# Kernel optimization log

Hardware: AMD Instinct MI355X
Metric: run time of the kernel (lower is better)

## Reference

```python
import jax, jax.numpy as jnp
import numpy as np

B, T = 512, 8192
DT = jnp.float32(1e-3)


def setup_inputs() -> dict:
    key = jax.random.key(0)
    k1, k2, k3, k4 = jax.random.split(key, 4)
    # scale noise so the 8192-step linear recurrence stays well-conditioned
    xicovs = jax.random.normal(k1, (B, T, 2, 2), jnp.float32) * 0.05
    dy = jax.random.normal(k2, (B, T, 2), jnp.float32) * 0.05
    coeffs_A = jax.random.uniform(k3, (2, 2), jnp.float32, -0.05, 0.05)  # 'uniform' init kernel
    C = jax.random.normal(k4, (2, 2), jnp.float32)
    return {"xicovs": xicovs, "dy": dy, "coeffs_A": coeffs_A, "C": C}


def reference(xicovs, dy, coeffs_A, C):
    # xicovs: [B,T,2,2], dy: [B,T,2]
    Bv = xicovs.shape[0]
    # initial state [1,0] broadcast over batch
    x0 = jnp.broadcast_to(jnp.array([1.0, 0.0], jnp.float32), (Bv, 2))
    xi_t = jnp.swapaxes(xicovs, 0, 1)  # [T,B,2,2]
    dy_t = jnp.swapaxes(dy, 0, 1)      # [T,B,2]

    def step(x, inp):
        xic, dyt = inp  # [B,2,2], [B,2]
        # cell emits C @ x_prev * dt
        out = jnp.einsum('ij,bj->bi', C, x) * DT
        A_minus_xiC = coeffs_A - jnp.einsum('bij,jk->bik', xic, C)  # [B,2,2]
        dx = jnp.einsum('bij,bj->bi', A_minus_xiC, x) * DT + jnp.einsum('bij,bj->bi', xic, dyt)
        return x + dx, out

    _, outs = jax.lax.scan(step, x0, (xi_t, dy_t))  # outs: [T,B,2]
    return jnp.swapaxes(outs, 0, 1)  # [B,T,2] (return_sequences=True)
```

## Files before the change

### kernel.cpp

```cpp
#include <hip/hip_runtime.h>


#define B_   512
#define T_   8192
#define LPT  8
#define NT   1024
#define NB   2
static_assert(NT * LPT == T_, "one block covers one batch");

#define SLICE_F4 128

struct Aff { float m00, m01, m10, m11, v0, v1; };

__device__ __forceinline__ Aff aff_compose(const Aff& L, const Aff& E) {
    Aff r;
    r.m00 = L.m00*E.m00 + L.m01*E.m10;
    r.m01 = L.m00*E.m01 + L.m01*E.m11;
    r.m10 = L.m10*E.m00 + L.m11*E.m10;
    r.m11 = L.m10*E.m01 + L.m11*E.m11;
    r.v0  = L.m00*E.v0  + L.m01*E.v1 + L.v0;
    r.v1  = L.m10*E.v0  + L.m11*E.v1 + L.v1;
    return r;
}

__device__ __forceinline__ Aff aff_identity() {
    Aff r; r.m00 = 1.f; r.m01 = 0.f; r.m10 = 0.f; r.m11 = 1.f; r.v0 = 0.f; r.v1 = 0.f;
    return r;
}

#define STEP_MAP(i, S)                                                  \
    {                                                                   \
        const float4 x4 = a[i];                                         \
        const float dyx = ((i)&1) ? d[(i)>>1].z : d[(i)>>1].x;          \
        const float dyy = ((i)&1) ? d[(i)>>1].w : d[(i)>>1].y;          \
        (S).m00 = i00 - (x4.x*cd00 + x4.y*cd10);                        \
        (S).m01 = i01 - (x4.x*cd01 + x4.y*cd11);                        \
        (S).m10 = i10 - (x4.z*cd00 + x4.w*cd10);                        \
        (S).m11 = i11 - (x4.z*cd01 + x4.w*cd11);                        \
        (S).v0  = x4.x*dyx + x4.y*dyy;                                  \
        (S).v1  = x4.z*dyx + x4.w*dyy;                                  \
    }

template<bool PREFETCH_DY>
__device__ __forceinline__ void process_batch(
    float4 (&t)[8], float4 (&u)[4],
    float4* __restrict__ slice, float4* __restrict__ lds4,
    const int lane, const int wave,
    const float cd00, const float cd01, const float cd10, const float cd11,
    const float i00, const float i01, const float i10, const float i11,
    float4* __restrict__ ow,
    const float4* __restrict__ dw_next, float4 (&u_next)[4])
{
    float4 a[LPT];
    #pragma unroll
    for (int r = 0; r < 4; ++r) {
        #pragma unroll
        for (int jj = 0; jj < 2; ++jj) {
            int j = 2*r + jj;
            int f = j*64 + lane;
            int rel = (f >> 3) & 15;
            slice[rel*8 + ((lane & 7) ^ (rel & 7))] = t[j];
        }
        if ((lane >> 4) == r) {
            int rel = lane & 15;
            #pragma unroll
            for (int s = 0; s < LPT; ++s)
                a[s] = slice[rel*8 + (s ^ (rel & 7))];
        }
    }

    float4 d[4];
    #pragma unroll
    for (int r = 0; r < 2; ++r) {
        #pragma unroll
        for (int jj = 0; jj < 2; ++jj) {
            int j = 2*r + jj;
            int f = j*64 + lane;
            int rel = (f >> 2) & 31;
            slice[rel*4 + ((lane & 3) ^ (rel & 3))] = u[j];
        }
        if ((lane >> 5) == r) {
            int rel = lane & 31;
            #pragma unroll
            for (int s = 0; s < 4; ++s)
                d[s] = slice[rel*4 + (s ^ (rel & 3))];
        }
    }

    Aff P;
    STEP_MAP(0, P);
    #pragma unroll
    for (int i = 1; i < LPT; ++i) { Aff s; STEP_MAP(i, s); P = aff_compose(s, P); }

    Aff S = P;
    #pragma unroll
    for (int sh = 1; sh < 64; sh <<= 1) {
        Aff q;
        q.m00 = __shfl_up(S.m00, sh); q.m01 = __shfl_up(S.m01, sh);
        q.m10 = __shfl_up(S.m10, sh); q.m11 = __shfl_up(S.m11, sh);
        q.v0  = __shfl_up(S.v0,  sh); q.v1  = __shfl_up(S.v1,  sh);
        if (lane >= sh) S = aff_compose(S, q);
    }

    if (lane == 63) {
        float* h = (float*)slice;
        h[0] = S.m00; h[1] = S.m01; h[2] = S.m10; h[3] = S.m11;
        h[4] = S.v0;  h[5] = S.v1;
    }
    __syncthreads();

    Aff Ew = aff_identity();
    for (int w = 0; w < wave; ++w) {
        const float* h = (const float*)(lds4 + w * SLICE_F4);
        Aff t2;
        t2.m00 = h[0]; t2.m01 = h[1]; t2.m10 = h[2]; t2.m11 = h[3];
        t2.v0  = h[4]; t2.v1  = h[5];
        Ew = aff_compose(t2, Ew);
    }
    __syncthreads();

    if constexpr (PREFETCH_DY) {
        #pragma unroll
        for (int j = 0; j < 4; ++j) u_next[j] = dw_next[j*64 + lane];
    }

    Aff El;
    El.m00 = __shfl_up(S.m00, 1); El.m01 = __shfl_up(S.m01, 1);
    El.m10 = __shfl_up(S.m10, 1); El.m11 = __shfl_up(S.m11, 1);
    El.v0  = __shfl_up(S.v0,  1); El.v1  = __shfl_up(S.v1,  1);
    if (lane == 0) El = aff_identity();

    Aff E = aff_compose(El, Ew);
    float x0 = E.m00 + E.v0;
    float x1 = E.m10 + E.v1;

    float4 o4[4];
    #pragma unroll
    for (int i = 0; i < LPT; ++i) {
        float oxx = cd00*x0 + cd01*x1;
        float oyy = cd10*x0 + cd11*x1;
        if (i & 1) { o4[i>>1].z = oxx; o4[i>>1].w = oyy; }
        else       { o4[i>>1].x = oxx; o4[i>>1].y = oyy; }
        Aff s; STEP_MAP(i, s);
        float nx0 = s.m00*x0 + s.m01*x1 + s.v0;
        float nx1 = s.m10*x0 + s.m11*x1 + s.v1;
        x0 = nx0; x1 = nx1;
    }

    #pragma unroll
    for (int r = 0; r < 2; ++r) {
        if ((lane >> 5) == r) {
            int rel = lane & 31;
            #pragma unroll
            for (int s = 0; s < 4; ++s)
                slice[rel*4 + (s ^ (rel & 3))] = o4[s];
        }
        #pragma unroll
        for (int jj = 0; jj < 2; ++jj) {
            int j = 2*r + jj;
            int f = j*64 + lane;
            int rel = (f >> 2) & 31;
            ow[f] = slice[rel*4 + ((lane & 3) ^ (rel & 3))];
        }
    }
}

__global__ __launch_bounds__(NT, 4) void grm_fused(
    const float* __restrict__ xic, const float* __restrict__ dy,
    const float* __restrict__ Aptr, const float* __restrict__ Cptr,
    float4* __restrict__ out4)
{
    __shared__ float4 lds4[16 * SLICE_F4];

    const int tid  = threadIdx.x;
    const int lane = tid & 63;
    const int wave = tid >> 6;

    float4* slice = lds4 + wave * SLICE_F4;

    const float DT = 1e-3f;
    const float cd00 = Cptr[0]*DT, cd01 = Cptr[1]*DT;
    const float cd10 = Cptr[2]*DT, cd11 = Cptr[3]*DT;
    const float i00 = 1.0f + Aptr[0]*DT, i01 = Aptr[1]*DT;
    const float i10 = Aptr[2]*DT,        i11 = 1.0f + Aptr[3]*DT;

    const int b0     = blockIdx.x * NB;
    const int wbase0 = b0 * T_ + wave * 512;
    const int wbase1 = wbase0 + T_;
    const float4* xw0 = (const float4*)xic + wbase0;
    const float4* dw0 = (const float4*)dy  + (wbase0 >> 1);
    float4*       ow0 = out4 + (wbase0 >> 1);
    const float4* xw1 = (const float4*)xic + wbase1;
    const float4* dw1 = (const float4*)dy  + (wbase1 >> 1);
    float4*       ow1 = out4 + (wbase1 >> 1);

    float4 t0[8], u0[4], t1[8], u1[4];
    #pragma unroll
    for (int j = 0; j < 8; ++j) t0[j] = xw0[j*64 + lane];
    #pragma unroll
    for (int j = 0; j < 4; ++j) u0[j] = dw0[j*64 + lane];
    #pragma unroll
    for (int j = 0; j < 8; ++j) t1[j] = xw1[j*64 + lane];

    process_batch<true>(t0, u0, slice, lds4, lane, wave,
                        cd00, cd01, cd10, cd11, i00, i01, i10, i11,
                        ow0, dw1, u1);

    process_batch<false>(t1, u1, slice, lds4, lane, wave,
                         cd00, cd01, cd10, cd11, i00, i01, i10, i11,
                         ow1, dw1, u1);
}

#undef STEP_MAP

extern "C" void kernel_launch(void* const* d_in, const int* in_sizes, int n_in,
                              void* d_out, int out_size, void* d_ws, size_t ws_size,
                              hipStream_t stream) {
    const float* xic  = (const float*)d_in[0];
    const float* dy   = (const float*)d_in[1];
    const float* Aptr = (const float*)d_in[2];
    const float* Cptr = (const float*)d_in[3];
    float4* out = (float4*)d_out;

    grm_fused<<<B_ / NB, NT, 0, stream>>>(xic, dy, Aptr, Cptr, out);
}
```

Baseline: 168.5 us.

## Stage next batch's xicovs into LDS with async global-to-LDS loads

The second batch's xicovs tile (7 of 8 float4 per lane) is now prefetched with `global_load_lds` into a new per-wave LDS staging buffer, instead of being held in registers across the first batch's computation. The aim is to cut register pressure while keeping the load in flight. The dy prefetch and the remaining xicovs float4 are moved to after the sequential output pass. This adds about 112 KB of LDS per block, which is fine at one block per CU. The later dy prefetch may expose more load latency, and correctness depends on the compiler inserting the right wait before the staged data is read back.

```diff
diff --git a/kernel.cpp b/kernel.cpp
--- a/kernel.cpp
+++ b/kernel.cpp
@@ -9,6 +9,7 @@
 static_assert(NT * LPT == T_, "one block covers one batch");
 
 #define SLICE_F4 128
+#define STAGE_F4 448
 
 struct Aff { float m00, m01, m10, m11, v0, v1; };
 
@@ -26,6 +27,13 @@
 __device__ __forceinline__ Aff aff_identity() {
     Aff r; r.m00 = 1.f; r.m01 = 0.f; r.m10 = 0.f; r.m11 = 1.f; r.v0 = 0.f; r.v1 = 0.f;
     return r;
+}
+
+__device__ __forceinline__ void glds16(const float4* g, float4* l) {
+    __builtin_amdgcn_global_load_lds(
+        (const __attribute__((address_space(1))) void*)g,
+        (__attribute__((address_space(3))) void*)l,
+        16, 0, 0);
 }
 
 #define STEP_MAP(i, S)                                                  \
@@ -41,15 +49,16 @@
         (S).v1  = x4.z*dyx + x4.w*dyy;                                  \
     }
 
-template<bool PREFETCH_DY>
+template<bool PREFETCH>
 __device__ __forceinline__ void process_batch(
     float4 (&t)[8], float4 (&u)[4],
-    float4* __restrict__ slice, float4* __restrict__ lds4,
+    float4* __restrict__ slice, float4* __restrict__ ldsw,
     const int lane, const int wave,
     const float cd00, const float cd01, const float cd10, const float cd11,
     const float i00, const float i01, const float i10, const float i11,
     float4* __restrict__ ow,
-    const float4* __restrict__ dw_next, float4 (&u_next)[4])
+    const float4* __restrict__ dw_next, float4 (&u_next)[4],
+    const float4* __restrict__ xtail_next, float4& ttail_next)
 {
     float4 a[LPT];
     #pragma unroll
@@ -111,18 +120,13 @@
 
     Aff Ew = aff_identity();
     for (int w = 0; w < wave; ++w) {
-        const float* h = (const float*)(lds4 + w * SLICE_F4);
+        const float* h = (const float*)(ldsw + w * SLICE_F4);
         Aff t2;
         t2.m00 = h[0]; t2.m01 = h[1]; t2.m10 = h[2]; t2.m11 = h[3];
         t2.v0  = h[4]; t2.v1  = h[5];
         Ew = aff_compose(t2, Ew);
     }
     __syncthreads();
-
-    if constexpr (PREFETCH_DY) {
-        #pragma unroll
-        for (int j = 0; j < 4; ++j) u_next[j] = dw_next[j*64 + lane];
-    }
 
     Aff El;
     El.m00 = __shfl_up(S.m00, 1); El.m01 = __shfl_up(S.m01, 1);
@@ -147,6 +151,12 @@
         x0 = nx0; x1 = nx1;
     }
 
+    if constexpr (PREFETCH) {
+        #pragma unroll
+        for (int j = 0; j < 4; ++j) u_next[j] = dw_next[j*64 + lane];
+        ttail_next = xtail_next[lane];
+    }
+
     #pragma unroll
     for (int r = 0; r < 2; ++r) {
         if ((lane >> 5) == r) {
@@ -170,13 +180,15 @@
     const float* __restrict__ Aptr, const float* __restrict__ Cptr,
     float4* __restrict__ out4)
 {
-    __shared__ float4 lds4[16 * SLICE_F4];
+    __shared__ float4 work [16 * SLICE_F4];
+    __shared__ float4 stage[16 * STAGE_F4];
 
     const int tid  = threadIdx.x;
     const int lane = tid & 63;
     const int wave = tid >> 6;
 
-    float4* slice = lds4 + wave * SLICE_F4;
+    float4* slice = work  + wave * SLICE_F4;
+    float4* stw   = stage + wave * STAGE_F4;
 
     const float DT = 1e-3f;
     const float cd00 = Cptr[0]*DT, cd01 = Cptr[1]*DT;
@@ -200,15 +212,18 @@
     #pragma unroll
     for (int j = 0; j < 4; ++j) u0[j] = dw0[j*64 + lane];
     #pragma unroll
-    for (int j = 0; j < 8; ++j) t1[j] = xw1[j*64 + lane];
-
-    process_batch<true>(t0, u0, slice, lds4, lane, wave,
+    for (int j = 0; j < 7; ++j) glds16(xw1 + j*64 + lane, stw + j*64);
+
+    process_batch<true>(t0, u0, slice, work, lane, wave,
                         cd00, cd01, cd10, cd11, i00, i01, i10, i11,
-                        ow0, dw1, u1);
-
-    process_batch<false>(t1, u1, slice, lds4, lane, wave,
+                        ow0, dw1, u1, xw1 + 7*64, t1[7]);
+
+    #pragma unroll
+    for (int j = 0; j < 7; ++j) t1[j] = stw[j*64 + lane];
+
+    process_batch<false>(t1, u1, slice, work, lane, wave,
                          cd00, cd01, cd10, cd11, i00, i01, i10, i11,
-                         ow1, dw1, u1);
+                         ow1, dw1, u1, xw1, t1[7]);
 }
 
 #undef STEP_MAP
```

Measured after the change: 165.1 us. 2.1% less time.
